# Kernel optimization log

Measured on AMD Instinct MI355X. Metric: run time of the kernel, lower is better.

The kernel has to match this reference:

```python
import jax, jax.numpy as jnp
import numpy as np

N_STREAMS = 4
HIDDEN = 1024
SINKHORN_ITERS = 20
TAU = 0.05
EPS = 1e-6
RMS_EPS = 1e-8


def rms_norm(x, weight):
    # x: [T, d] fp32
    rms = jnp.mean(x * x, axis=-1, keepdims=True)
    return x * jax.lax.rsqrt(rms + RMS_EPS) * weight


def sinkhorn_log(logits, n_iters=SINKHORN_ITERS, tau=TAU):
    # logits: [T, n, n] -> doubly-stochastic [T, n, n]
    Z = logits / tau
    u0 = jnp.zeros(Z.shape[:-1], Z.dtype)  # [T, n]
    v0 = jnp.zeros_like(u0)

    def body(i, uv):
        u, v = uv
        u = -jax.nn.logsumexp(Z + v[..., None, :], axis=-1)
        v = -jax.nn.logsumexp(Z + u[..., :, None], axis=-2)
        return (u, v)

    u, v = jax.lax.fori_loop(0, n_iters, body, (u0, v0))
    return jnp.exp(Z + u[..., :, None] + v[..., None, :])


def setup_inputs() -> dict:
    key = jax.random.key(0)
    ks = jax.random.split(key, 6)
    d = N_STREAMS * HIDDEN
    x_streams = jax.random.normal(ks[0], (4, 2048, N_STREAMS, HIDDEN), dtype=jnp.float32)
    scale = 1.0 / np.sqrt(d)
    return {
        "x_streams": x_streams,
        "rms_weight": jnp.ones((d,), jnp.float32),
        "W_pre": jax.random.normal(ks[1], (N_STREAMS, d), jnp.float32) * scale,
        "W_post": jax.random.normal(ks[2], (N_STREAMS, d), jnp.float32) * scale,
        "W_res": jax.random.normal(ks[3], (N_STREAMS * N_STREAMS, d), jnp.float32) * scale,
        "bias_pre": jnp.zeros((N_STREAMS,), jnp.float32),
        "bias_post": jnp.zeros((N_STREAMS,), jnp.float32),
        "bias_res": jnp.zeros((N_STREAMS * N_STREAMS,), jnp.float32),
        "alpha_pre": jnp.full((1,), 0.01, jnp.float32),
        "alpha_post": jnp.full((1,), 0.01, jnp.float32),
        "alpha_res": jnp.full((1,), 0.01, jnp.float32),
        "W_sub": jax.random.normal(ks[4], (HIDDEN, HIDDEN), jnp.float32) * (1.0 / np.sqrt(HIDDEN)),
    }


def reference(x_streams, rms_weight, W_pre, W_post, W_res, bias_pre, bias_post,
              bias_res, alpha_pre, alpha_post, alpha_res, W_sub):
    B, S, n, C = x_streams.shape
    d = n * C
    x_flat = x_streams.reshape(B * S, d).astype(jnp.float32)
    x_norm = rms_norm(x_flat, rms_weight)

    H_pre = jax.nn.sigmoid(alpha_pre * (x_norm @ W_pre.T) + bias_pre)        # [T, n]
    H_post = 2.0 * jax.nn.sigmoid(alpha_post * (x_norm @ W_post.T) + bias_post)
    H_res = sinkhorn_log((alpha_res * (x_norm @ W_res.T) + bias_res).reshape(B * S, n, n))

    H_pre = H_pre.reshape(B, S, n)
    H_post = H_post.reshape(B, S, n)
    H_res = H_res.reshape(B, S, n, n)

    H_pre_w = H_pre / (jnp.sum(H_pre, axis=-1, keepdims=True) + EPS)
    H_post_w = H_post / (jnp.sum(H_post, axis=-1, keepdims=True) + EPS)

    # pre-aggregate streams -> single stream
    x_layer = jnp.einsum('bsnc,bsn->bsc', x_streams, H_pre_w)
    # sublayer: bias-free linear
    y = x_layer @ W_sub.T                                                    # [B, S, C]
    # broadcast sublayer output back to streams
    y_expanded = H_post_w[..., None] * y[:, :, None, :]                      # [B, S, n, C]
    # doubly-stochastic residual stream mixing
    x_mixed = jnp.einsum('bsic,bsoi->bsoc', x_streams, H_res)
    return x_mixed + y_expanded
```

## Files before the change

### kernel.cpp

```cpp
#include <hip/hip_runtime.h>

#define NTOK 8192
#define D 4096
#define CH 1024

typedef __attribute__((ext_vector_type(8))) short short8v;
typedef __attribute__((ext_vector_type(4))) float float4v;
typedef __attribute__((ext_vector_type(4))) unsigned short ushort4v;
typedef __attribute__((ext_vector_type(8))) unsigned short ushort8v;

static __device__ __forceinline__ unsigned short f2bf(float f) {
  unsigned int u = __float_as_uint(f);
  u += 0x7fff + ((u >> 16) & 1);
  return (unsigned short)(u >> 16);
}

static __device__ __forceinline__ float bf2f(unsigned short u) {
  return __uint_as_float(((unsigned int)u) << 16);
}

static __device__ __forceinline__ void async_cp16(const void* g, void* l) {
  __builtin_amdgcn_global_load_lds((__attribute__((address_space(1))) void*)g,
                                   (__attribute__((address_space(3))) void*)l,
                                   16, 0, 0);
}

__global__ __launch_bounds__(256) void prep_kernel(
    const float* __restrict__ Wpre, const float* __restrict__ Wpost,
    const float* __restrict__ Wres, const float* __restrict__ rms_w,
    const float* __restrict__ Wsub, unsigned short* __restrict__ Wg,
    unsigned short* __restrict__ Wb) {
  const int bid = blockIdx.x;
  if (bid < 2048) {
    int i = bid * 512 + threadIdx.x * 2;
    float2 v = *(const float2*)(Wsub + i);
    unsigned int packed = (unsigned int)f2bf(v.x) | ((unsigned int)f2bf(v.y) << 16);
    *(unsigned int*)(Wb + i) = packed;
  } else {
    int j = (bid - 2048) * 512 + threadIdx.x * 2;
    int g = j >> 12;
    int k = j & 4095;
    float2 r = *(const float2*)(rms_w + k);
    float2 wv;
    if (g < 4)       wv = *(const float2*)(Wpre + g * 4096 + k);
    else if (g < 8)  wv = *(const float2*)(Wpost + (g - 4) * 4096 + k);
    else if (g < 24) wv = *(const float2*)(Wres + (g - 8) * 4096 + k);
    else             { wv.x = 0.f; wv.y = 0.f; }
    unsigned int packed = (unsigned int)f2bf(wv.x * r.x) |
                          ((unsigned int)f2bf(wv.y * r.y) << 16);
    *(unsigned int*)(Wg + g * 4096 + k) = packed;
  }
}

__global__ __launch_bounds__(512, 4) void gates_kernel(
    const float* __restrict__ x, const unsigned short* __restrict__ Wg,
    const float* __restrict__ bpre, const float* __restrict__ bpost,
    const float* __restrict__ bres, const float* __restrict__ apre,
    const float* __restrict__ apost, const float* __restrict__ ares,
    float* __restrict__ gates_out, unsigned short* __restrict__ xlayer) {
  __shared__ __align__(16) unsigned short xb[8][4096];
  __shared__ float pl[8][8][32];
  __shared__ float sqp[8][8];
  __shared__ float logits_lds[8][32];
  __shared__ float sq_lds[8];
  __shared__ float s_lds[8];
  __shared__ float hpre_lds[8][4];

  const int tid = threadIdx.x;
  const int lane = tid & 63;
  const int w = tid >> 6;
  const int tok0 = blockIdx.x * 8;

  {
    float sqw[8];
    const float* src0 = x + (size_t)tok0 * D + w * 512 + lane * 8;
    const int gslot = w * 64 + lane;
#pragma unroll
    for (int t = 0; t < 8; ++t) {
      const float* s = src0 + (size_t)t * D;
      float4 a4 = *(const float4*)s;
      float4 b4 = *(const float4*)(s + 4);
      sqw[t] = a4.x * a4.x + a4.y * a4.y + a4.z * a4.z + a4.w * a4.w +
               b4.x * b4.x + b4.y * b4.y + b4.z * b4.z + b4.w * b4.w;
      ushort8v p;
      p[0] = f2bf(a4.x); p[1] = f2bf(a4.y); p[2] = f2bf(a4.z); p[3] = f2bf(a4.w);
      p[4] = f2bf(b4.x); p[5] = f2bf(b4.y); p[6] = f2bf(b4.z); p[7] = f2bf(b4.w);
      *(ushort8v*)(&xb[t][(gslot ^ t) * 8]) = p;
    }
#pragma unroll
    for (int t = 0; t < 8; ++t) {
      float v = sqw[t];
      for (int off = 32; off > 0; off >>= 1) v += __shfl_xor(v, off, 64);
      if (lane == 0) sqp[w][t] = v;
    }
  }

  float4v acc0 = {0.f, 0.f, 0.f, 0.f};
  float4v acc1 = {0.f, 0.f, 0.f, 0.f};
  {
    const int arow = lane & 7;
    const int apos = lane >> 4;
    const unsigned short* bb0 =
        Wg + (size_t)(lane & 15) * D + w * 512 + apos * 8;
    const unsigned short* bb1 = bb0 + 16 * D;
#pragma unroll 4
    for (int ks = 0; ks < 16; ++ks) {
      short8v a = *(const short8v*)(
          &xb[arow][((w * 64 + ks * 4 + apos) ^ arow) * 8]);
      short8v b0 = *(const short8v*)(bb0 + ks * 32);
      short8v b1 = *(const short8v*)(bb1 + ks * 32);
      acc0 = __builtin_amdgcn_mfma_f32_16x16x32_bf16(a, b0, acc0, 0, 0, 0);
      acc1 = __builtin_amdgcn_mfma_f32_16x16x32_bf16(a, b1, acc1, 0, 0, 0);
    }
  }

  if (lane < 32) {
    const int tr = (lane >> 4) * 4;
    const int gc = lane & 15;
#pragma unroll
    for (int r = 0; r < 4; ++r) {
      pl[w][tr + r][gc] = acc0[r];
      pl[w][tr + r][16 + gc] = acc1[r];
    }
  }
  __syncthreads();

  if (tid < 256) {
    const int t = tid >> 5, g = tid & 31;
    float v = 0.f;
#pragma unroll
    for (int ww = 0; ww < 8; ++ww) v += pl[ww][t][g];
    logits_lds[t][g] = v;
  } else if (tid < 264) {
    const int t = tid - 256;
    float v = 0.f;
#pragma unroll
    for (int ww = 0; ww < 8; ++ww) v += sqp[ww][t];
    sq_lds[t] = v;
  }
  __syncthreads();

  if (tid < 8) {
    const int t = tid;
    float s = rsqrtf(sq_lds[t] * (1.0f / 4096.0f) + 1e-8f);
    s_lds[t] = s;
    float a_pre = apre[0], a_post = apost[0];

    float hp[4];
    float sum_p = 1e-6f;
#pragma unroll
    for (int i = 0; i < 4; ++i) {
      float z = a_pre * (s * logits_lds[t][i]) + bpre[i];
      hp[i] = 1.0f / (1.0f + __expf(-z));
      sum_p += hp[i];
    }
    float inv_p = 1.0f / sum_p;
#pragma unroll
    for (int i = 0; i < 4; ++i) hpre_lds[t][i] = hp[i] * inv_p;

    float* go = gates_out + (size_t)(tok0 + t) * 20;
    float hq[4];
    float sum_q = 1e-6f;
#pragma unroll
    for (int i = 0; i < 4; ++i) {
      float z = a_post * (s * logits_lds[t][4 + i]) + bpost[i];
      hq[i] = 2.0f / (1.0f + __expf(-z));
      sum_q += hq[i];
    }
    float inv_q = 1.0f / sum_q;
#pragma unroll
    for (int i = 0; i < 4; ++i) go[i] = hq[i] * inv_q;
  }
  __syncthreads();

  auto phB = [&](int sI) {
    const int t = sI >> 8;
    const int c4 = (sI & 255) * 4;
    const int bi = t * 4096 + (((c4 >> 3) ^ t) << 3) + (c4 & 7);
    const unsigned short* xr = &xb[0][0];
    const float h0 = hpre_lds[t][0], h1 = hpre_lds[t][1];
    const float h2 = hpre_lds[t][2], h3 = hpre_lds[t][3];
    ushort4v v0 = *(const ushort4v*)(xr + bi);
    ushort4v v1 = *(const ushort4v*)(xr + bi + 1024);
    ushort4v v2 = *(const ushort4v*)(xr + bi + 2048);
    ushort4v v3 = *(const ushort4v*)(xr + bi + 3072);
    ushort4v o;
    o.x = f2bf(h0 * bf2f(v0.x) + h1 * bf2f(v1.x) + h2 * bf2f(v2.x) + h3 * bf2f(v3.x));
    o.y = f2bf(h0 * bf2f(v0.y) + h1 * bf2f(v1.y) + h2 * bf2f(v2.y) + h3 * bf2f(v3.y));
    o.z = f2bf(h0 * bf2f(v0.z) + h1 * bf2f(v1.z) + h2 * bf2f(v2.z) + h3 * bf2f(v3.z));
    o.w = f2bf(h0 * bf2f(v0.w) + h1 * bf2f(v1.w) + h2 * bf2f(v2.w) + h3 * bf2f(v3.w));
    *(ushort4v*)(xlayer + (size_t)(tok0 + t) * CH + c4) = o;
  };

  if (w == 0) {
    if (lane < 32) {
      const int t = lane >> 2;
      const int r = lane & 3;
      const float s = s_lds[t];
      const float a_res = ares[0];
      float Zrow[4], Zcol[4];
#pragma unroll
      for (int j = 0; j < 4; ++j) {
        Zrow[j] = (a_res * (s * logits_lds[t][8 + r * 4 + j]) + bres[r * 4 + j]) * 20.0f;
        Zcol[j] = (a_res * (s * logits_lds[t][8 + j * 4 + r]) + bres[j * 4 + r]) * 20.0f;
      }
      float u = 0.f, v = 0.f;
      const int base = t << 2;
      for (int it = 0; it < 20; ++it) {
        float v0 = __shfl(v, base + 0, 64), v1 = __shfl(v, base + 1, 64);
        float v2 = __shfl(v, base + 2, 64), v3 = __shfl(v, base + 3, 64);
        float a0 = Zrow[0] + v0, a1 = Zrow[1] + v1, a2 = Zrow[2] + v2, a3 = Zrow[3] + v3;
        float m = fmaxf(fmaxf(a0, a1), fmaxf(a2, a3));
        float sm = __expf(a0 - m) + __expf(a1 - m) + __expf(a2 - m) + __expf(a3 - m);
        u = -(m + __logf(sm));
        float u0 = __shfl(u, base + 0, 64), u1 = __shfl(u, base + 1, 64);
        float u2 = __shfl(u, base + 2, 64), u3 = __shfl(u, base + 3, 64);
        float b0 = Zcol[0] + u0, b1 = Zcol[1] + u1, b2 = Zcol[2] + u2, b3 = Zcol[3] + u3;
        float m2 = fmaxf(fmaxf(b0, b1), fmaxf(b2, b3));
        float sm2 = __expf(b0 - m2) + __expf(b1 - m2) + __expf(b2 - m2) + __expf(b3 - m2);
        v = -(m2 + __logf(sm2));
      }
      float v0 = __shfl(v, base + 0, 64), v1 = __shfl(v, base + 1, 64);
      float v2 = __shfl(v, base + 2, 64), v3 = __shfl(v, base + 3, 64);
      float* go = gates_out + (size_t)(tok0 + t) * 20;
      go[4 + r * 4 + 0] = __expf(Zrow[0] + u + v0);
      go[4 + r * 4 + 1] = __expf(Zrow[1] + u + v1);
      go[4 + r * 4 + 2] = __expf(Zrow[2] + u + v2);
      go[4 + r * 4 + 3] = __expf(Zrow[3] + u + v3);
    }
#pragma unroll
    for (int i = 0; i < 4; ++i) phB(1792 + i * 64 + lane);
  } else {
    const int b = tid - 64;
#pragma unroll
    for (int i = 0; i < 4; ++i) phB(b + i * 448);
  }
}

__global__ __launch_bounds__(256, 2) void gemm_epi(
    const unsigned short* __restrict__ A,
    const unsigned short* __restrict__ B,
    const float* __restrict__ x,
    const float* __restrict__ gates,
    float* __restrict__ out) {
  __shared__ __align__(16) unsigned short stg[32768];
  __shared__ float hpost_sm[128][4];
  __shared__ float hres_sm[128][16];

  const int tid = threadIdx.x;
  const int lane = tid & 63;
  const int w = tid >> 6;
  const int n0 = blockIdx.x * 128;
  const int m0 = blockIdx.y * 128;

  {
    const int r = tid >> 1, half = tid & 1;
    const float* gp = gates + (size_t)(m0 + r) * 20 + half * 10;
#pragma unroll
    for (int j = 0; j < 10; ++j) {
      int jj = half * 10 + j;
      float v = gp[j];
      if (jj < 4) hpost_sm[r][jj] = v;
      else        hres_sm[r][jj - 4] = v;
    }
  }

  float4v accf[4][4];
#pragma unroll
  for (int mi = 0; mi < 4; ++mi)
#pragma unroll
    for (int ni = 0; ni < 4; ++ni) {
      accf[mi][ni].x = 0.f; accf[mi][ni].y = 0.f;
      accf[mi][ni].z = 0.f; accf[mi][ni].w = 0.f;
    }

  const int wm = (w >> 1) * 64;
  const int wn = (w & 1) * 64;
  const int srow = lane >> 3;
  const int sslot = lane & 7;

#define STAGE(KT, BUF)                                                        \
  {                                                                           \
    const int k0s = (KT) * 64;                                                \
    unsigned short* As = stg + (BUF) * 8192;                                  \
    unsigned short* Bs = stg + 16384 + (BUF) * 8192;                          \
    _Pragma("unroll")                                                         \
    for (int i = 0; i < 4; ++i) {                                             \
      int chunk = w * 4 + i;                                                  \
      int row = chunk * 8 + srow;                                             \
      int qg = sslot ^ (row & 7);                                             \
      async_cp16(A + (size_t)(m0 + row) * 1024 + k0s + qg * 8,                \
                 (void*)(As + chunk * 512));                                  \
      async_cp16(B + (size_t)(n0 + row) * 1024 + k0s + qg * 8,                \
                 (void*)(Bs + chunk * 512));                                  \
    }                                                                         \
  }

  STAGE(0, 0);
  __syncthreads();

  for (int kt = 0; kt < 16; ++kt) {
    const int cur = kt & 1;
    if (kt < 15) STAGE(kt + 1, cur ^ 1);
    const unsigned short* As = stg + cur * 8192;
    const unsigned short* Bs = stg + 16384 + cur * 8192;
#pragma unroll
    for (int kk = 0; kk < 2; ++kk) {
      short8v a[4], b[4];
#pragma unroll
      for (int mi = 0; mi < 4; ++mi) {
        int row = wm + mi * 16 + (lane & 15);
        int q = (kk * 4 + (lane >> 4)) ^ (row & 7);
        a[mi] = *(const short8v*)(As + row * 64 + q * 8);
      }
#pragma unroll
      for (int ni = 0; ni < 4; ++ni) {
        int row = wn + ni * 16 + (lane & 15);
        int q = (kk * 4 + (lane >> 4)) ^ (row & 7);
        b[ni] = *(const short8v*)(Bs + row * 64 + q * 8);
      }
#pragma unroll
      for (int mi = 0; mi < 4; ++mi)
#pragma unroll
        for (int ni = 0; ni < 4; ++ni)
          accf[mi][ni] = __builtin_amdgcn_mfma_f32_16x16x32_bf16(
              a[mi], b[ni], accf[mi][ni], 0, 0, 0);
    }
    __syncthreads();
  }

  const int rg = (lane >> 4) * 4;
  const int cl = lane & 15;
#pragma unroll
  for (int mi = 0; mi < 4; ++mi) {
#pragma unroll
    for (int r = 0; r < 4; ++r) {
      const int row = wm + mi * 16 + rg + r;
      const size_t t = (size_t)(m0 + row);
      const float4 hq = *(const float4*)(&hpost_sm[row][0]);
      const float4 h0 = *(const float4*)(&hres_sm[row][0]);
      const float4 h1 = *(const float4*)(&hres_sm[row][4]);
      const float4 h2 = *(const float4*)(&hres_sm[row][8]);
      const float4 h3 = *(const float4*)(&hres_sm[row][12]);
      const float* xp = x + t * 4096 + n0 + wn + cl;
      float* op = out + t * 4096 + n0 + wn + cl;
#pragma unroll
      for (int ni = 0; ni < 4; ++ni) {
        const int c = ni * 16;
        float x0 = xp[c], x1 = xp[c + 1024], x2 = xp[c + 2048], x3 = xp[c + 3072];
        float y = accf[mi][ni][r];
        op[c]        = x0 * h0.x + x1 * h0.y + x2 * h0.z + x3 * h0.w + hq.x * y;
        op[c + 1024] = x0 * h1.x + x1 * h1.y + x2 * h1.z + x3 * h1.w + hq.y * y;
        op[c + 2048] = x0 * h2.x + x1 * h2.y + x2 * h2.z + x3 * h2.w + hq.z * y;
        op[c + 3072] = x0 * h3.x + x1 * h3.y + x2 * h3.z + x3 * h3.w + hq.w * y;
      }
    }
  }
}

extern "C" void kernel_launch(void* const* d_in, const int* in_sizes, int n_in,
                              void* d_out, int out_size, void* d_ws, size_t ws_size,
                              hipStream_t stream) {
  const float* x     = (const float*)d_in[0];
  const float* rms_w = (const float*)d_in[1];
  const float* Wpre  = (const float*)d_in[2];
  const float* Wpost = (const float*)d_in[3];
  const float* Wres  = (const float*)d_in[4];
  const float* bpre  = (const float*)d_in[5];
  const float* bpost = (const float*)d_in[6];
  const float* bres  = (const float*)d_in[7];
  const float* apre  = (const float*)d_in[8];
  const float* apost = (const float*)d_in[9];
  const float* ares  = (const float*)d_in[10];
  const float* Wsub  = (const float*)d_in[11];
  float* out = (float*)d_out;

  char* ws = (char*)d_ws;
  float* gates           = (float*)ws;
  unsigned short* Wb     = (unsigned short*)(ws + (1 << 20));
  unsigned short* Wg     = (unsigned short*)(ws + (3 << 20));
  unsigned short* xlayer = (unsigned short*)(ws + (4 << 20));

  prep_kernel<<<2304, 256, 0, stream>>>(Wpre, Wpost, Wres, rms_w, Wsub, Wg, Wb);
  gates_kernel<<<1024, 512, 0, stream>>>(x, Wg, bpre, bpost, bres,
                                         apre, apost, ares, gates, xlayer);
  gemm_epi<<<dim3(8, 64), 256, 0, stream>>>(xlayer, Wb, x, gates, out);
}
```

Measured before the change: 350.1 us.

## Shrink gates kernel LDS with two-phase K loop and vectorize GEMM epilogue via LDS

The gates kernel drops to 256 threads. Each wave now handles two 512-wide K chunks through a small per-wave LDS buffer, prefetching the second chunk into registers while the first chunk's MFMAs run. This cuts LDS use sharply, so more blocks can be resident. The xlayer aggregation now re-reads x from global memory in fp32 instead of reusing the bf16 LDS copy, which also changes rounding slightly. The GEMM epilogue stages accumulators through LDS so each thread issues float4 loads and stores of x and out instead of scalar strided accesses, at the cost of extra LDS traffic and waits.

```diff
diff --git a/kernel.cpp b/kernel.cpp
--- a/kernel.cpp
+++ b/kernel.cpp
@@ -52,17 +52,16 @@
   }
 }
 
-__global__ __launch_bounds__(512, 4) void gates_kernel(
+__global__ __launch_bounds__(256, 4) void gates_kernel(
     const float* __restrict__ x, const unsigned short* __restrict__ Wg,
     const float* __restrict__ bpre, const float* __restrict__ bpost,
     const float* __restrict__ bres, const float* __restrict__ apre,
     const float* __restrict__ apost, const float* __restrict__ ares,
     float* __restrict__ gates_out, unsigned short* __restrict__ xlayer) {
-  __shared__ __align__(16) unsigned short xb[8][4096];
-  __shared__ float pl[8][8][32];
-  __shared__ float sqp[8][8];
+  __shared__ __align__(16) unsigned short xb[4][8][512];
+  __shared__ float pl[4][8][32];
+  __shared__ float sqp[4][8];
   __shared__ float logits_lds[8][32];
-  __shared__ float sq_lds[8];
   __shared__ float s_lds[8];
   __shared__ float hpre_lds[8][4];
 
@@ -71,49 +70,79 @@
   const int w = tid >> 6;
   const int tok0 = blockIdx.x * 8;
 
+  const float* src = x + (size_t)tok0 * D + w * 1024 + lane * 8;
+  float sqacc[8];
+
   {
-    float sqw[8];
-    const float* src0 = x + (size_t)tok0 * D + w * 512 + lane * 8;
-    const int gslot = w * 64 + lane;
+    float4 A0[8], B0[8];
 #pragma unroll
     for (int t = 0; t < 8; ++t) {
-      const float* s = src0 + (size_t)t * D;
-      float4 a4 = *(const float4*)s;
-      float4 b4 = *(const float4*)(s + 4);
-      sqw[t] = a4.x * a4.x + a4.y * a4.y + a4.z * a4.z + a4.w * a4.w +
-               b4.x * b4.x + b4.y * b4.y + b4.z * b4.z + b4.w * b4.w;
+      A0[t] = *(const float4*)(src + (size_t)t * D);
+      B0[t] = *(const float4*)(src + (size_t)t * D + 4);
+    }
+#pragma unroll
+    for (int t = 0; t < 8; ++t) {
+      sqacc[t] = A0[t].x * A0[t].x + A0[t].y * A0[t].y + A0[t].z * A0[t].z +
+                 A0[t].w * A0[t].w + B0[t].x * B0[t].x + B0[t].y * B0[t].y +
+                 B0[t].z * B0[t].z + B0[t].w * B0[t].w;
       ushort8v p;
-      p[0] = f2bf(a4.x); p[1] = f2bf(a4.y); p[2] = f2bf(a4.z); p[3] = f2bf(a4.w);
-      p[4] = f2bf(b4.x); p[5] = f2bf(b4.y); p[6] = f2bf(b4.z); p[7] = f2bf(b4.w);
-      *(ushort8v*)(&xb[t][(gslot ^ t) * 8]) = p;
-    }
-#pragma unroll
-    for (int t = 0; t < 8; ++t) {
-      float v = sqw[t];
-      for (int off = 32; off > 0; off >>= 1) v += __shfl_xor(v, off, 64);
-      if (lane == 0) sqp[w][t] = v;
-    }
-  }
+      p[0] = f2bf(A0[t].x); p[1] = f2bf(A0[t].y); p[2] = f2bf(A0[t].z); p[3] = f2bf(A0[t].w);
+      p[4] = f2bf(B0[t].x); p[5] = f2bf(B0[t].y); p[6] = f2bf(B0[t].z); p[7] = f2bf(B0[t].w);
+      *(ushort8v*)(&xb[w][t][(lane ^ t) * 8]) = p;
+    }
+  }
+
+  float4 A1[8], B1[8];
+#pragma unroll
+  for (int t = 0; t < 8; ++t) {
+    A1[t] = *(const float4*)(src + (size_t)t * D + 512);
+    B1[t] = *(const float4*)(src + (size_t)t * D + 516);
+  }
+  asm volatile("s_waitcnt lgkmcnt(0)" ::: "memory");
 
   float4v acc0 = {0.f, 0.f, 0.f, 0.f};
   float4v acc1 = {0.f, 0.f, 0.f, 0.f};
-  {
-    const int arow = lane & 7;
-    const int apos = lane >> 4;
-    const unsigned short* bb0 =
-        Wg + (size_t)(lane & 15) * D + w * 512 + apos * 8;
-    const unsigned short* bb1 = bb0 + 16 * D;
-#pragma unroll 4
-    for (int ks = 0; ks < 16; ++ks) {
-      short8v a = *(const short8v*)(
-          &xb[arow][((w * 64 + ks * 4 + apos) ^ arow) * 8]);
-      short8v b0 = *(const short8v*)(bb0 + ks * 32);
-      short8v b1 = *(const short8v*)(bb1 + ks * 32);
-      acc0 = __builtin_amdgcn_mfma_f32_16x16x32_bf16(a, b0, acc0, 0, 0, 0);
-      acc1 = __builtin_amdgcn_mfma_f32_16x16x32_bf16(a, b1, acc1, 0, 0, 0);
-    }
-  }
-
+  const int arow = lane & 7;
+  const int apos = lane >> 4;
+  const unsigned short* bb0 = Wg + (size_t)(lane & 15) * D + w * 1024 + apos * 8;
+  const unsigned short* bb1 = bb0 + 16 * D;
+
+#pragma unroll
+  for (int ks = 0; ks < 16; ++ks) {
+    short8v a = *(const short8v*)(&xb[w][arow][((ks * 4 + apos) ^ arow) * 8]);
+    short8v b0v = *(const short8v*)(bb0 + ks * 32);
+    short8v b1v = *(const short8v*)(bb1 + ks * 32);
+    acc0 = __builtin_amdgcn_mfma_f32_16x16x32_bf16(a, b0v, acc0, 0, 0, 0);
+    acc1 = __builtin_amdgcn_mfma_f32_16x16x32_bf16(a, b1v, acc1, 0, 0, 0);
+  }
+
+#pragma unroll
+  for (int t = 0; t < 8; ++t) {
+    sqacc[t] += A1[t].x * A1[t].x + A1[t].y * A1[t].y + A1[t].z * A1[t].z +
+                A1[t].w * A1[t].w + B1[t].x * B1[t].x + B1[t].y * B1[t].y +
+                B1[t].z * B1[t].z + B1[t].w * B1[t].w;
+    ushort8v p;
+    p[0] = f2bf(A1[t].x); p[1] = f2bf(A1[t].y); p[2] = f2bf(A1[t].z); p[3] = f2bf(A1[t].w);
+    p[4] = f2bf(B1[t].x); p[5] = f2bf(B1[t].y); p[6] = f2bf(B1[t].z); p[7] = f2bf(B1[t].w);
+    *(ushort8v*)(&xb[w][t][(lane ^ t) * 8]) = p;
+  }
+  asm volatile("s_waitcnt lgkmcnt(0)" ::: "memory");
+
+#pragma unroll
+  for (int ks = 0; ks < 16; ++ks) {
+    short8v a = *(const short8v*)(&xb[w][arow][((ks * 4 + apos) ^ arow) * 8]);
+    short8v b0v = *(const short8v*)(bb0 + 512 + ks * 32);
+    short8v b1v = *(const short8v*)(bb1 + 512 + ks * 32);
+    acc0 = __builtin_amdgcn_mfma_f32_16x16x32_bf16(a, b0v, acc0, 0, 0, 0);
+    acc1 = __builtin_amdgcn_mfma_f32_16x16x32_bf16(a, b1v, acc1, 0, 0, 0);
+  }
+
+#pragma unroll
+  for (int t = 0; t < 8; ++t) {
+    float v = sqacc[t];
+    for (int off = 32; off > 0; off >>= 1) v += __shfl_xor(v, off, 64);
+    if (lane == 0) sqp[w][t] = v;
+  }
   if (lane < 32) {
     const int tr = (lane >> 4) * 4;
     const int gc = lane & 15;
@@ -125,24 +154,16 @@
   }
   __syncthreads();
 
-  if (tid < 256) {
+  {
     const int t = tid >> 5, g = tid & 31;
-    float v = 0.f;
-#pragma unroll
-    for (int ww = 0; ww < 8; ++ww) v += pl[ww][t][g];
-    logits_lds[t][g] = v;
-  } else if (tid < 264) {
-    const int t = tid - 256;
-    float v = 0.f;
-#pragma unroll
-    for (int ww = 0; ww < 8; ++ww) v += sqp[ww][t];
-    sq_lds[t] = v;
+    logits_lds[t][g] = pl[0][t][g] + pl[1][t][g] + pl[2][t][g] + pl[3][t][g];
   }
   __syncthreads();
 
   if (tid < 8) {
     const int t = tid;
-    float s = rsqrtf(sq_lds[t] * (1.0f / 4096.0f) + 1e-8f);
+    float sq = sqp[0][t] + sqp[1][t] + sqp[2][t] + sqp[3][t];
+    float s = rsqrtf(sq * (1.0f / 4096.0f) + 1e-8f);
     s_lds[t] = s;
     float a_pre = apre[0], a_post = apost[0];
 
@@ -173,67 +194,57 @@
   }
   __syncthreads();
 
-  auto phB = [&](int sI) {
-    const int t = sI >> 8;
-    const int c4 = (sI & 255) * 4;
-    const int bi = t * 4096 + (((c4 >> 3) ^ t) << 3) + (c4 & 7);
-    const unsigned short* xr = &xb[0][0];
+  if (w == 0 && lane < 32) {
+    const int t = lane >> 2;
+    const int r = lane & 3;
+    const float s = s_lds[t];
+    const float a_res = ares[0];
+    float Zrow[4], Zcol[4];
+#pragma unroll
+    for (int j = 0; j < 4; ++j) {
+      Zrow[j] = (a_res * (s * logits_lds[t][8 + r * 4 + j]) + bres[r * 4 + j]) * 20.0f;
+      Zcol[j] = (a_res * (s * logits_lds[t][8 + j * 4 + r]) + bres[j * 4 + r]) * 20.0f;
+    }
+    float u = 0.f, v = 0.f;
+    const int base = t << 2;
+    for (int it = 0; it < 20; ++it) {
+      float v0 = __shfl(v, base + 0, 64), v1 = __shfl(v, base + 1, 64);
+      float v2 = __shfl(v, base + 2, 64), v3 = __shfl(v, base + 3, 64);
+      float a0 = Zrow[0] + v0, a1 = Zrow[1] + v1, a2 = Zrow[2] + v2, a3 = Zrow[3] + v3;
+      float m = fmaxf(fmaxf(a0, a1), fmaxf(a2, a3));
+      float sm = __expf(a0 - m) + __expf(a1 - m) + __expf(a2 - m) + __expf(a3 - m);
+      u = -(m + __logf(sm));
+      float u0 = __shfl(u, base + 0, 64), u1 = __shfl(u, base + 1, 64);
+      float u2 = __shfl(u, base + 2, 64), u3 = __shfl(u, base + 3, 64);
+      float b0 = Zcol[0] + u0, b1 = Zcol[1] + u1, b2 = Zcol[2] + u2, b3 = Zcol[3] + u3;
+      float m2 = fmaxf(fmaxf(b0, b1), fmaxf(b2, b3));
+      float sm2 = __expf(b0 - m2) + __expf(b1 - m2) + __expf(b2 - m2) + __expf(b3 - m2);
+      v = -(m2 + __logf(sm2));
+    }
+    float v0 = __shfl(v, base + 0, 64), v1 = __shfl(v, base + 1, 64);
+    float v2 = __shfl(v, base + 2, 64), v3 = __shfl(v, base + 3, 64);
+    float* go = gates_out + (size_t)(tok0 + t) * 20;
+    go[4 + r * 4 + 0] = __expf(Zrow[0] + u + v0);
+    go[4 + r * 4 + 1] = __expf(Zrow[1] + u + v1);
+    go[4 + r * 4 + 2] = __expf(Zrow[2] + u + v2);
+    go[4 + r * 4 + 3] = __expf(Zrow[3] + u + v3);
+  }
+
+#pragma unroll 2
+  for (int t = 0; t < 8; ++t) {
     const float h0 = hpre_lds[t][0], h1 = hpre_lds[t][1];
     const float h2 = hpre_lds[t][2], h3 = hpre_lds[t][3];
-    ushort4v v0 = *(const ushort4v*)(xr + bi);
-    ushort4v v1 = *(const ushort4v*)(xr + bi + 1024);
-    ushort4v v2 = *(const ushort4v*)(xr + bi + 2048);
-    ushort4v v3 = *(const ushort4v*)(xr + bi + 3072);
+    const size_t xbase = (size_t)(tok0 + t) * D + tid * 4;
+    float4 x0 = *(const float4*)(x + xbase);
+    float4 x1 = *(const float4*)(x + xbase + 1024);
+    float4 x2 = *(const float4*)(x + xbase + 2048);
+    float4 x3 = *(const float4*)(x + xbase + 3072);
     ushort4v o;
-    o.x = f2bf(h0 * bf2f(v0.x) + h1 * bf2f(v1.x) + h2 * bf2f(v2.x) + h3 * bf2f(v3.x));
-    o.y = f2bf(h0 * bf2f(v0.y) + h1 * bf2f(v1.y) + h2 * bf2f(v2.y) + h3 * bf2f(v3.y));
-    o.z = f2bf(h0 * bf2f(v0.z) + h1 * bf2f(v1.z) + h2 * bf2f(v2.z) + h3 * bf2f(v3.z));
-    o.w = f2bf(h0 * bf2f(v0.w) + h1 * bf2f(v1.w) + h2 * bf2f(v2.w) + h3 * bf2f(v3.w));
-    *(ushort4v*)(xlayer + (size_t)(tok0 + t) * CH + c4) = o;
-  };
-
-  if (w == 0) {
-    if (lane < 32) {
-      const int t = lane >> 2;
-      const int r = lane & 3;
-      const float s = s_lds[t];
-      const float a_res = ares[0];
-      float Zrow[4], Zcol[4];
-#pragma unroll
-      for (int j = 0; j < 4; ++j) {
-        Zrow[j] = (a_res * (s * logits_lds[t][8 + r * 4 + j]) + bres[r * 4 + j]) * 20.0f;
-        Zcol[j] = (a_res * (s * logits_lds[t][8 + j * 4 + r]) + bres[j * 4 + r]) * 20.0f;
-      }
-      float u = 0.f, v = 0.f;
-      const int base = t << 2;
-      for (int it = 0; it < 20; ++it) {
-        float v0 = __shfl(v, base + 0, 64), v1 = __shfl(v, base + 1, 64);
-        float v2 = __shfl(v, base + 2, 64), v3 = __shfl(v, base + 3, 64);
-        float a0 = Zrow[0] + v0, a1 = Zrow[1] + v1, a2 = Zrow[2] + v2, a3 = Zrow[3] + v3;
-        float m = fmaxf(fmaxf(a0, a1), fmaxf(a2, a3));
-        float sm = __expf(a0 - m) + __expf(a1 - m) + __expf(a2 - m) + __expf(a3 - m);
-        u = -(m + __logf(sm));
-        float u0 = __shfl(u, base + 0, 64), u1 = __shfl(u, base + 1, 64);
-        float u2 = __shfl(u, base + 2, 64), u3 = __shfl(u, base + 3, 64);
-        float b0 = Zcol[0] + u0, b1 = Zcol[1] + u1, b2 = Zcol[2] + u2, b3 = Zcol[3] + u3;
-        float m2 = fmaxf(fmaxf(b0, b1), fmaxf(b2, b3));
-        float sm2 = __expf(b0 - m2) + __expf(b1 - m2) + __expf(b2 - m2) + __expf(b3 - m2);
-        v = -(m2 + __logf(sm2));
-      }
-      float v0 = __shfl(v, base + 0, 64), v1 = __shfl(v, base + 1, 64);
-      float v2 = __shfl(v, base + 2, 64), v3 = __shfl(v, base + 3, 64);
-      float* go = gates_out + (size_t)(tok0 + t) * 20;
-      go[4 + r * 4 + 0] = __expf(Zrow[0] + u + v0);
-      go[4 + r * 4 + 1] = __expf(Zrow[1] + u + v1);
-      go[4 + r * 4 + 2] = __expf(Zrow[2] + u + v2);
-      go[4 + r * 4 + 3] = __expf(Zrow[3] + u + v3);
-    }
-#pragma unroll
-    for (int i = 0; i < 4; ++i) phB(1792 + i * 64 + lane);
-  } else {
-    const int b = tid - 64;
-#pragma unroll
-    for (int i = 0; i < 4; ++i) phB(b + i * 448);
+    o.x = f2bf(h0 * x0.x + h1 * x1.x + h2 * x2.x + h3 * x3.x);
+    o.y = f2bf(h0 * x0.y + h1 * x1.y + h2 * x2.y + h3 * x3.y);
+    o.z = f2bf(h0 * x0.z + h1 * x1.z + h2 * x2.z + h3 * x3.z);
+    o.w = f2bf(h0 * x0.w + h1 * x1.w + h2 * x2.w + h3 * x3.w);
+    *(ushort4v*)(xlayer + (size_t)(tok0 + t) * CH + tid * 4) = o;
   }
 }
 
@@ -329,32 +340,59 @@
     __syncthreads();
   }
 
+  float* mysc = (float*)stg + w * 1088;
   const int rg = (lane >> 4) * 4;
   const int cl = lane & 15;
+  const int erow = lane >> 2;
+  const int ec = lane & 3;
 #pragma unroll
   for (int mi = 0; mi < 4; ++mi) {
 #pragma unroll
-    for (int r = 0; r < 4; ++r) {
-      const int row = wm + mi * 16 + rg + r;
-      const size_t t = (size_t)(m0 + row);
-      const float4 hq = *(const float4*)(&hpost_sm[row][0]);
-      const float4 h0 = *(const float4*)(&hres_sm[row][0]);
-      const float4 h1 = *(const float4*)(&hres_sm[row][4]);
-      const float4 h2 = *(const float4*)(&hres_sm[row][8]);
-      const float4 h3 = *(const float4*)(&hres_sm[row][12]);
-      const float* xp = x + t * 4096 + n0 + wn + cl;
-      float* op = out + t * 4096 + n0 + wn + cl;
-#pragma unroll
-      for (int ni = 0; ni < 4; ++ni) {
-        const int c = ni * 16;
-        float x0 = xp[c], x1 = xp[c + 1024], x2 = xp[c + 2048], x3 = xp[c + 3072];
-        float y = accf[mi][ni][r];
-        op[c]        = x0 * h0.x + x1 * h0.y + x2 * h0.z + x3 * h0.w + hq.x * y;
-        op[c + 1024] = x0 * h1.x + x1 * h1.y + x2 * h1.z + x3 * h1.w + hq.y * y;
-        op[c + 2048] = x0 * h2.x + x1 * h2.y + x2 * h2.z + x3 * h2.w + hq.z * y;
-        op[c + 3072] = x0 * h3.x + x1 * h3.y + x2 * h3.z + x3 * h3.w + hq.w * y;
-      }
-    }
+    for (int ni = 0; ni < 4; ++ni)
+#pragma unroll
+      for (int r = 0; r < 4; ++r)
+        mysc[(rg + r) * 68 + ni * 16 + cl] = accf[mi][ni][r];
+    asm volatile("s_waitcnt lgkmcnt(0)" ::: "memory");
+
+    const int row128 = wm + mi * 16 + erow;
+    const size_t t = (size_t)(m0 + row128);
+    const float4 hq = *(const float4*)(&hpost_sm[row128][0]);
+    const float4 h0 = *(const float4*)(&hres_sm[row128][0]);
+    const float4 h1 = *(const float4*)(&hres_sm[row128][4]);
+    const float4 h2 = *(const float4*)(&hres_sm[row128][8]);
+    const float4 h3 = *(const float4*)(&hres_sm[row128][12]);
+#pragma unroll
+    for (int s = 0; s < 4; ++s) {
+      const int c4 = ec + s * 4;
+      float4 y4 = *(const float4*)(&mysc[erow * 68 + c4 * 4]);
+      const size_t xb_ = t * 4096 + n0 + wn + c4 * 4;
+      float4 x0 = *(const float4*)(x + xb_);
+      float4 x1 = *(const float4*)(x + xb_ + 1024);
+      float4 x2 = *(const float4*)(x + xb_ + 2048);
+      float4 x3 = *(const float4*)(x + xb_ + 3072);
+      float4 rr;
+      rr.x = x0.x * h0.x + x1.x * h0.y + x2.x * h0.z + x3.x * h0.w + hq.x * y4.x;
+      rr.y = x0.y * h0.x + x1.y * h0.y + x2.y * h0.z + x3.y * h0.w + hq.x * y4.y;
+      rr.z = x0.z * h0.x + x1.z * h0.y + x2.z * h0.z + x3.z * h0.w + hq.x * y4.z;
+      rr.w = x0.w * h0.x + x1.w * h0.y + x2.w * h0.z + x3.w * h0.w + hq.x * y4.w;
+      *(float4*)(out + xb_) = rr;
+      rr.x = x0.x * h1.x + x1.x * h1.y + x2.x * h1.z + x3.x * h1.w + hq.y * y4.x;
+      rr.y = x0.y * h1.x + x1.y * h1.y + x2.y * h1.z + x3.y * h1.w + hq.y * y4.y;
+      rr.z = x0.z * h1.x + x1.z * h1.y + x2.z * h1.z + x3.z * h1.w + hq.y * y4.z;
+      rr.w = x0.w * h1.x + x1.w * h1.y + x2.w * h1.z + x3.w * h1.w + hq.y * y4.w;
+      *(float4*)(out + xb_ + 1024) = rr;
+      rr.x = x0.x * h2.x + x1.x * h2.y + x2.x * h2.z + x3.x * h2.w + hq.z * y4.x;
+      rr.y = x0.y * h2.x + x1.y * h2.y + x2.y * h2.z + x3.y * h2.w + hq.z * y4.y;
+      rr.z = x0.z * h2.x + x1.z * h2.y + x2.z * h2.z + x3.z * h2.w + hq.z * y4.z;
+      rr.w = x0.w * h2.x + x1.w * h2.y + x2.w * h2.z + x3.w * h2.w + hq.z * y4.w;
+      *(float4*)(out + xb_ + 2048) = rr;
+      rr.x = x0.x * h3.x + x1.x * h3.y + x2.x * h3.z + x3.x * h3.w + hq.w * y4.x;
+      rr.y = x0.y * h3.x + x1.y * h3.y + x2.y * h3.z + x3.y * h3.w + hq.w * y4.y;
+      rr.z = x0.z * h3.x + x1.z * h3.y + x2.z * h3.z + x3.z * h3.w + hq.w * y4.z;
+      rr.w = x0.w * h3.x + x1.w * h3.y + x2.w * h3.z + x3.w * h3.w + hq.w * y4.w;
+      *(float4*)(out + xb_ + 3072) = rr;
+    }
+    asm volatile("s_waitcnt lgkmcnt(0)" ::: "memory");
   }
 }
 
@@ -382,7 +420,7 @@
   unsigned short* xlayer = (unsigned short*)(ws + (4 << 20));
 
   prep_kernel<<<2304, 256, 0, stream>>>(Wpre, Wpost, Wres, rms_w, Wsub, Wg, Wb);
-  gates_kernel<<<1024, 512, 0, stream>>>(x, Wg, bpre, bpost, bres,
+  gates_kernel<<<1024, 256, 0, stream>>>(x, Wg, bpre, bpost, bres,
                                          apre, apost, ares, gates, xlayer);
   gemm_epi<<<dim3(8, 64), 256, 0, stream>>>(xlayer, Wb, x, gates, out);
 }
```

Measured after the change: 445.1 us. +27.1%, slower.
